# Optimization experiments

Measured on AMD Instinct MI355X. Metric: run time of the kernel, lower is better.

## Reference

```python
import jax, jax.numpy as jnp
import numpy as np

B, T, C = 2, 512, 128
H = 4 * C
EPS_LN = 1e-5
EPS_WKV = 1e-6


def setup_inputs() -> dict:
    key = jax.random.key(0)
    ks = jax.random.split(key, 12)
    def rn(i, shape, s):
        return jax.random.normal(ks[i], shape, jnp.float32) * s
    return {
        "x": jax.random.normal(ks[0], (B, T, C), jnp.float32),
        "ln1_g": jnp.ones((C,), jnp.float32), "ln1_b": jnp.zeros((C,), jnp.float32),
        "mu": rn(1, (C,), 0.1),
        "Wr": rn(2, (C, C), 0.02), "br": jnp.zeros((C,), jnp.float32),
        "Wk": rn(3, (C, C), 0.02), "bk": jnp.zeros((C,), jnp.float32),
        "Wv": rn(4, (C, C), 0.02), "bv": jnp.zeros((C,), jnp.float32),
        "w_decay": rn(5, (C,), 0.5),
        "Wo": rn(6, (C, C), 0.02), "bo": jnp.zeros((C,), jnp.float32),
        "ln2_g": jnp.ones((C,), jnp.float32), "ln2_b": jnp.zeros((C,), jnp.float32),
        "W1": rn(7, (C, H), 0.02), "b1": jnp.zeros((H,), jnp.float32),
        "W2": rn(8, (H, C), 0.02), "b2": jnp.zeros((C,), jnp.float32),
    }


def _ln(x, g, b):
    m = x.mean(-1, keepdims=True)
    v = ((x - m) ** 2).mean(-1, keepdims=True)
    return (x - m) * jax.lax.rsqrt(v + EPS_LN) * g + b


def _wkv_dir(k, v, w_lc):
    # k, v: (B,T,C); w_lc: (T,C) per-(position,channel) decay weight
    p = k[:, :, None, :] * w_lc[None, None, :, :]              # (B,T,L,C)
    p = jnp.exp(p - jax.lax.stop_gradient(p.max(-1, keepdims=True)))  # stable, max over C (as in source, dim=-1)
    p = p / (p.sum(-1, keepdims=True) + EPS_WKV)               # normalize over channel dim, as written in torch
    return jnp.einsum('btlc,blc->btc', p, v)


def _forward(x, ln1_g, ln1_b, mu, Wr, br, Wk, bk, Wv, bv, w_decay, Wo, bo, ln2_g, ln2_b, W1, b1, W2, b2):
    Tn = x.shape[1]
    h = _ln(x, ln1_g, ln1_b)
    # TemporalShift: past half shifted right, future half shifted left
    xp, xf = jnp.split(h, 2, axis=-1)
    xp = jnp.pad(xp, ((0, 0), (1, 0), (0, 0)))[:, :-1]
    xf = jnp.pad(xf, ((0, 0), (0, 1), (0, 0)))[:, 1:]
    hs = h + mu * jnp.concatenate([xp, xf], axis=-1)
    r = jax.nn.sigmoid(hs @ Wr + br)
    k = hs @ Wk + bk
    v = hs @ Wv + bv
    t = jnp.arange(Tn, dtype=x.dtype)[:, None]                 # (T,1)
    neg_w = -jnp.exp(w_decay)[None, :]                         # (1,C)
    w_f = neg_w * (Tn - 1 - t) / (Tn - 1)                      # (T,C)
    w_b = neg_w * t / (Tn - 1)                                 # (T,C)
    x_f = _wkv_dir(k, v, w_f)
    x_b = jnp.flip(_wkv_dir(jnp.flip(k, 1), jnp.flip(v, 1), w_b), 1)
    wk = r * (x_f + x_b) * 0.5
    y = x + wk @ Wo + bo
    h2 = _ln(y, ln2_g, ln2_b)
    m = jax.nn.gelu(h2 @ W1 + b1, approximate=False) @ W2 + b2
    return y + m


def reference(x, ln1_g, ln1_b, mu, Wr, br, Wk, bk, Wv, bv, w_decay, Wo, bo, ln2_g, ln2_b, W1, b1, W2, b2):
    return _forward(x, ln1_g, ln1_b, mu, Wr, br, Wk, bk, Wv, bv, w_decay, Wo, bo, ln2_g, ln2_b, W1, b1, W2, b2)
```

## Files before the change

kernel.cpp:

```cpp
#include <hip/hip_runtime.h>
#include <hip/hip_bf16.h>

#define Bq 2
#define Tq 512
#define Cq 128
#define Hq 512
#define NROW (Bq*Tq)

__device__ __forceinline__ float bfbits2f(unsigned short u) {
    return __uint_as_float(((unsigned)u) << 16);
}
__device__ __forceinline__ bool detect_f32(const void* sent) {
    return *(const unsigned*)sent == 0x3F800000u;
}
#define LD(p, i) (f32 ? ((const float*)(p))[i] : bfbits2f(((const unsigned short*)(p))[i]))
__device__ __forceinline__ float4 LD4(const void* p, int i, bool f32) {
    if (f32) return ((const float4*)p)[i >> 2];
    ushort4 u = *(const ushort4*)((const unsigned short*)p + i);
    return make_float4(bfbits2f(u.x), bfbits2f(u.y), bfbits2f(u.z), bfbits2f(u.w));
}

__global__ __launch_bounds__(512) void kA_qkv(
    const void* __restrict__ sent,
    const void* __restrict__ x,
    const void* __restrict__ ln1g, const void* __restrict__ ln1b,
    const void* __restrict__ mu,
    const void* __restrict__ Wr, const void* __restrict__ br,
    const void* __restrict__ Wk, const void* __restrict__ bk,
    const void* __restrict__ Wv, const void* __restrict__ bv,
    const void* __restrict__ wdec,
    float* __restrict__ r_out, float* __restrict__ u_out,
    float* __restrict__ v_out)
{
    const bool f32 = detect_f32(sent);
    int R0 = blockIdx.x * 2, tid = threadIdx.x;
    int g = tid >> 7, col = tid & 127;
    int t0 = R0 & (Tq - 1);
    int bbase = R0 - t0;

    __shared__ float h4[4][Cq];
    __shared__ __align__(16) float hsi[Cq][2];
    __shared__ __align__(16) float part[3][4][Cq][2];
    __shared__ float wred[8][2];

    {
        int t = t0 - 1 + g;
        int tcl = min(max(t, 0), Tq - 1);
        int row = bbase + tcl;
        float xv = LD(x, row * Cq + col);
        float s1 = xv, s2 = xv * xv;
        for (int off = 32; off; off >>= 1) {
            s1 += __shfl_xor(s1, off);
            s2 += __shfl_xor(s2, off);
        }
        int wid = tid >> 6;
        if ((tid & 63) == 0) { wred[wid][0] = s1; wred[wid][1] = s2; }
        __syncthreads();
        float S1 = wred[2 * g][0] + wred[2 * g + 1][0];
        float S2 = wred[2 * g][1] + wred[2 * g + 1][1];
        float m  = S1 * (1.f / Cq);
        float va = S2 * (1.f / Cq) - m * m;
        float rs = rsqrtf(va + 1e-5f);
        h4[g][col] = (xv - m) * rs * LD(ln1g, col) + LD(ln1b, col);
    }
    __syncthreads();

    if (g < 2) {
        int r2 = g, tt = t0 + r2;
        float hv = h4[r2 + 1][col];
        float nb;
        if (col < Cq / 2) nb = (tt > 0)      ? h4[r2][col]     : 0.f;
        else              nb = (tt < Tq - 1) ? h4[r2 + 2][col] : 0.f;
        hsi[col][r2] = hv + LD(mu, col) * nb;
    }
    __syncthreads();

    if (g < 3) {
        const void* W = (g == 0) ? Wr : (g == 1) ? Wk : Wv;
        int ks = (tid >> 5) & 3, j0 = (tid & 31) * 4;
        float a00 = 0.f, a01 = 0.f, a02 = 0.f, a03 = 0.f;
        float a10 = 0.f, a11 = 0.f, a12 = 0.f, a13 = 0.f;
        int c0 = ks * 32;
#pragma unroll 4
        for (int cc = c0; cc < c0 + 32; ++cc) {
            float4 w  = LD4(W, cc * Cq + j0, f32);
            float2 hv = *(const float2*)&hsi[cc][0];
            a00 += hv.x * w.x; a01 += hv.x * w.y; a02 += hv.x * w.z; a03 += hv.x * w.w;
            a10 += hv.y * w.x; a11 += hv.y * w.y; a12 += hv.y * w.z; a13 += hv.y * w.w;
        }
        *(float4*)&part[g][ks][j0][0]     = make_float4(a00, a10, a01, a11);
        *(float4*)&part[g][ks][j0 + 2][0] = make_float4(a02, a12, a03, a13);
    }
    __syncthreads();

    if (g < 3) {
#pragma unroll
        for (int r2 = 0; r2 < 2; ++r2) {
            float a = (part[g][0][col][r2] + part[g][1][col][r2])
                    + (part[g][2][col][r2] + part[g][3][col][r2]);
            int row = R0 + r2;
            if (g == 0) {
                float rr = 1.f / (1.f + __expf(-(a + LD(br, col))));
                r_out[row * Cq + col] = rr;
            } else if (g == 1) {
                float wd = LD(wdec, col);
                wd = fminf(fmaxf(wd, -20.f), 20.f);
                float negw = -__expf(wd);
                float uu = (a + LD(bk, col)) * negw;
                uu = fminf(fmaxf(uu, -30.f), 30.f);
                u_out[row * Cq + col] = uu;
            } else {
                v_out[row * Cq + col] = a + LD(bv, col);
            }
        }
    }
}

__global__ __launch_bounds__(512) void kB_wkv_ffn(
    const void* __restrict__ sent,
    const float* __restrict__ u_in,
    const float* __restrict__ v_in,
    const float* __restrict__ r_in,
    const void* __restrict__ x,
    const void* __restrict__ Wo, const void* __restrict__ bo,
    const void* __restrict__ lng, const void* __restrict__ lnb,
    const void* __restrict__ W1, const void* __restrict__ b1,
    const void* __restrict__ W2, const void* __restrict__ b2,
    void* __restrict__ out)
{
    const bool f32 = detect_f32(sent);
    int R0 = blockIdx.x * 2, tid = threadIdx.x;
    int b = R0 >> 9;
    const float inv511 = 1.f / (float)(Tq - 1);

    __shared__ float u2[2][Cq];
    __shared__ __align__(16) float rinv2[Tq][2];
    __shared__ float part[8][2][Cq];
    __shared__ __align__(16) float wki[Cq][2];
    __shared__ __align__(16) float h2i[Cq][2];
    __shared__ __align__(16) float m1i[Hq][2];
    __shared__ __align__(16) float pbuf[16 * Cq * 2];
    __shared__ float wred[8][2];

    if (tid < 256) u2[tid >> 7][tid & 127] = u_in[(R0 + (tid >> 7)) * Cq + (tid & 127)];
    __syncthreads();

    {
        int l = tid;
        float a = (float)(Tq - 1 - l) * inv511 * 1.44269504f;
#pragma unroll
        for (int r = 0; r < 2; ++r) {
            float s0 = 0.f, s1 = 0.f, s2 = 0.f, s3 = 0.f;
            const float4* uu4 = (const float4*)u2[r];
            for (int cc = 0; cc < Cq / 4; ++cc) {
                float4 uv = uu4[cc];
                s0 += exp2f(a * uv.x);
                s1 += exp2f(a * uv.y);
                s2 += exp2f(a * uv.z);
                s3 += exp2f(a * uv.w);
            }
            rinv2[l][r] = 1.f / ((s0 + s1) + (s2 + s3) + 1e-6f);
        }
    }
    __syncthreads();

    {
        int seg = tid >> 6, cp = tid & 63, c2 = cp * 2;
        float u00 = u2[0][c2], u01 = u2[0][c2 + 1];
        float u10 = u2[1][c2], u11 = u2[1][c2 + 1];
        float jb = (float)(seg * 64);
        float e00 = __expf(u00 * jb * inv511), e01 = __expf(u01 * jb * inv511);
        float e10 = __expf(u10 * jb * inv511), e11 = __expf(u11 * jb * inv511);
        float g00 = __expf(u00 * inv511), g01 = __expf(u01 * inv511);
        float g10 = __expf(u10 * inv511), g11 = __expf(u11 * inv511);
        float G00 = g00 * g00, G01 = g01 * g01, G10 = g10 * g10, G11 = g11 * g11;
        float p00 = 0.f, p01 = 0.f, p10 = 0.f, p11 = 0.f;
        float q00 = 0.f, q01 = 0.f, q10 = 0.f, q11 = 0.f;
        const float2* vb = (const float2*)(v_in + (size_t)b * Tq * Cq) + cp;
        int j0 = seg * 64;
        for (int j = j0; j < j0 + 64; j += 2) {
            int l = (Tq - 1) - j;
            float2 v0 = vb[(size_t)l * 64];
            float2 v1 = vb[(size_t)(l - 1) * 64];
            float2 ra = *(const float2*)&rinv2[l][0];
            float2 rb = *(const float2*)&rinv2[l - 1][0];
            p00 += v0.x * (e00 * ra.x); p01 += v0.y * (e01 * ra.x);
            p10 += v0.x * (e10 * ra.y); p11 += v0.y * (e11 * ra.y);
            q00 += v1.x * ((e00 * g00) * rb.x); q01 += v1.y * ((e01 * g01) * rb.x);
            q10 += v1.x * ((e10 * g10) * rb.y); q11 += v1.y * ((e11 * g11) * rb.y);
            e00 *= G00; e01 *= G01; e10 *= G10; e11 *= G11;
        }
        part[seg][0][c2]     = p00 + q00;
        part[seg][0][c2 + 1] = p01 + q01;
        part[seg][1][c2]     = p10 + q10;
        part[seg][1][c2 + 1] = p11 + q11;
    }
    __syncthreads();

    if (tid < 256) {
        int r = tid >> 7, c = tid & 127;
        float acc = ((part[0][r][c] + part[1][r][c]) + (part[2][r][c] + part[3][r][c]))
                  + ((part[4][r][c] + part[5][r][c]) + (part[6][r][c] + part[7][r][c]));
        wki[c][r] = r_in[(R0 + r) * Cq + c] * acc;
    }
    __syncthreads();

    {
        int ks = tid >> 5, c0 = (tid & 31) * 4;
        float a00 = 0.f, a01 = 0.f, a02 = 0.f, a03 = 0.f;
        float a10 = 0.f, a11 = 0.f, a12 = 0.f, a13 = 0.f;
        int k0 = ks * 8;
#pragma unroll
        for (int cc = k0; cc < k0 + 8; ++cc) {
            float4 w   = LD4(Wo, cc * Cq + c0, f32);
            float2 wk2 = *(const float2*)&wki[cc][0];
            a00 += wk2.x * w.x; a01 += wk2.x * w.y; a02 += wk2.x * w.z; a03 += wk2.x * w.w;
            a10 += wk2.y * w.x; a11 += wk2.y * w.y; a12 += wk2.y * w.z; a13 += wk2.y * w.w;
        }
        *(float4*)&pbuf[(ks * Cq + c0) * 2]     = make_float4(a00, a10, a01, a11);
        *(float4*)&pbuf[(ks * Cq + c0 + 2) * 2] = make_float4(a02, a12, a03, a13);
    }
    __syncthreads();

    float yv = 0.f;
    if (tid < 256) {
        int r = tid >> 7, c = tid & 127;
        float s = 0.f;
#pragma unroll
        for (int ks = 0; ks < 16; ++ks) s += pbuf[(ks * Cq + c) * 2 + r];
        yv = LD(x, (R0 + r) * Cq + c) + s + LD(bo, c);
    }
    {
        float s1 = yv, s2 = yv * yv;
        for (int off = 32; off; off >>= 1) {
            s1 += __shfl_xor(s1, off);
            s2 += __shfl_xor(s2, off);
        }
        int wid = tid >> 6;
        if ((tid & 63) == 0) { wred[wid][0] = s1; wred[wid][1] = s2; }
        __syncthreads();
        if (tid < 256) {
            int r = tid >> 7, c = tid & 127;
            float S1 = wred[2 * r][0] + wred[2 * r + 1][0];
            float S2 = wred[2 * r][1] + wred[2 * r + 1][1];
            float m  = S1 * (1.f / Cq);
            float va = S2 * (1.f / Cq) - m * m;
            float rs = rsqrtf(va + 1e-5f);
            h2i[c][r] = (yv - m) * rs * LD(lng, c) + LD(lnb, c);
        }
    }
    __syncthreads();

    {
        int ks = tid >> 7, j0 = (tid & 127) * 4;
        float a00 = 0.f, a01 = 0.f, a02 = 0.f, a03 = 0.f;
        float a10 = 0.f, a11 = 0.f, a12 = 0.f, a13 = 0.f;
        int c0 = ks * 32;
#pragma unroll 4
        for (int cc = c0; cc < c0 + 32; ++cc) {
            float4 w  = LD4(W1, cc * Hq + j0, f32);
            float2 hv = *(const float2*)&h2i[cc][0];
            a00 += hv.x * w.x; a01 += hv.x * w.y; a02 += hv.x * w.z; a03 += hv.x * w.w;
            a10 += hv.y * w.x; a11 += hv.y * w.y; a12 += hv.y * w.z; a13 += hv.y * w.w;
        }
        *(float4*)&pbuf[(ks * Hq + j0) * 2]     = make_float4(a00, a10, a01, a11);
        *(float4*)&pbuf[(ks * Hq + j0 + 2) * 2] = make_float4(a02, a12, a03, a13);
    }
    __syncthreads();
    {
        int j = tid;
        float bb = LD(b1, j);
        float x0 = ((pbuf[(0 * Hq + j) * 2]     + pbuf[(1 * Hq + j) * 2])
                  + (pbuf[(2 * Hq + j) * 2]     + pbuf[(3 * Hq + j) * 2])) + bb;
        float x1 = ((pbuf[(0 * Hq + j) * 2 + 1] + pbuf[(1 * Hq + j) * 2 + 1])
                  + (pbuf[(2 * Hq + j) * 2 + 1] + pbuf[(3 * Hq + j) * 2 + 1])) + bb;
        m1i[j][0] = 0.5f * x0 * (1.f + erff(x0 * 0.70710678f));
        m1i[j][1] = 0.5f * x1 * (1.f + erff(x1 * 0.70710678f));
    }
    __syncthreads();

    {
        int ks = tid >> 5, c0 = (tid & 31) * 4;
        float a00 = 0.f, a01 = 0.f, a02 = 0.f, a03 = 0.f;
        float a10 = 0.f, a11 = 0.f, a12 = 0.f, a13 = 0.f;
        int h0 = ks * 32;
#pragma unroll 4
        for (int hh = h0; hh < h0 + 32; ++hh) {
            float4 w  = LD4(W2, hh * Cq + c0, f32);
            float2 mv = *(const float2*)&m1i[hh][0];
            a00 += mv.x * w.x; a01 += mv.x * w.y; a02 += mv.x * w.z; a03 += mv.x * w.w;
            a10 += mv.y * w.x; a11 += mv.y * w.y; a12 += mv.y * w.z; a13 += mv.y * w.w;
        }
        __syncthreads();
        *(float4*)&pbuf[(ks * Cq + c0) * 2]     = make_float4(a00, a10, a01, a11);
        *(float4*)&pbuf[(ks * Cq + c0 + 2) * 2] = make_float4(a02, a12, a03, a13);
    }
    __syncthreads();
    if (tid < 256) {
        int r = tid >> 7, c = tid & 127;
        float s = 0.f;
#pragma unroll
        for (int ks = 0; ks < 16; ++ks) s += pbuf[(ks * Cq + c) * 2 + r];
        float val = yv + s + LD(b2, c);
        int idx = (R0 + r) * Cq + c;
        if (f32) ((float*)out)[idx] = val;
        else     ((__hip_bfloat16*)out)[idx] = __float2bfloat16(val);
    }
}

extern "C" void kernel_launch(void* const* d_in, const int* in_sizes, int n_in,
                              void* d_out, int out_size, void* d_ws, size_t ws_size,
                              hipStream_t stream)
{
    const void* x    = d_in[0];
    const void* ln1g = d_in[1];
    const void* ln1b = d_in[2];
    const void* mu   = d_in[3];
    const void* Wr   = d_in[4];
    const void* br   = d_in[5];
    const void* Wk   = d_in[6];
    const void* bk   = d_in[7];
    const void* Wv   = d_in[8];
    const void* bv   = d_in[9];
    const void* wdec = d_in[10];
    const void* Wo   = d_in[11];
    const void* bo   = d_in[12];
    const void* ln2g = d_in[13];
    const void* ln2b = d_in[14];
    const void* W1   = d_in[15];
    const void* b1   = d_in[16];
    const void* W2   = d_in[17];
    const void* b2   = d_in[18];

    float* ws = (float*)d_ws;
    float* u  = ws;
    float* r  = ws + 131072;
    float* v  = ws + 262144;

    kA_qkv<<<NROW / 2, 512, 0, stream>>>(ln1g, x, ln1g, ln1b, mu, Wr, br, Wk, bk, Wv, bv, wdec, r, u, v);
    kB_wkv_ffn<<<NROW / 2, 512, 0, stream>>>(ln1g, u, v, r, x, Wo, bo, ln2g, ln2b, W1, b1, W2, b2, d_out);
}
```

Baseline: 156.3 us.

## Remap WKV work per wavefront to drop block barriers and shuffle-reduce QKV

In the WKV+FFN kernel, each wavefront now loads its own copy of u and computes the normalizer rows (in reversed order) that it later consumes itself. This removes two block-wide barriers. The time-scan loop is unrolled by four, and the r and x loads are issued early so their latency overlaps the scan. In the QKV kernel, the partial-sum shared buffer and one barrier are replaced by a wave-level shuffle reduction with float4 bias and stores, and each wave handles one matrix and one row. The cost is redundant u loads per wave and fewer active waves (6 of 8) in the projection stage.

```diff
diff --git a/kernel.cpp b/kernel.cpp
--- a/kernel.cpp
+++ b/kernel.cpp
@@ -40,7 +40,6 @@
 
     __shared__ float h4[4][Cq];
     __shared__ __align__(16) float hsi[Cq][2];
-    __shared__ __align__(16) float part[3][4][Cq][2];
     __shared__ float wred[8][2];
 
     {
@@ -75,42 +74,66 @@
     }
     __syncthreads();
 
-    if (g < 3) {
-        const void* W = (g == 0) ? Wr : (g == 1) ? Wk : Wv;
-        int ks = (tid >> 5) & 3, j0 = (tid & 31) * 4;
-        float a00 = 0.f, a01 = 0.f, a02 = 0.f, a03 = 0.f;
-        float a10 = 0.f, a11 = 0.f, a12 = 0.f, a13 = 0.f;
-        int c0 = ks * 32;
-#pragma unroll 4
-        for (int cc = c0; cc < c0 + 32; ++cc) {
-            float4 w  = LD4(W, cc * Cq + j0, f32);
-            float2 hv = *(const float2*)&hsi[cc][0];
-            a00 += hv.x * w.x; a01 += hv.x * w.y; a02 += hv.x * w.z; a03 += hv.x * w.w;
-            a10 += hv.y * w.x; a11 += hv.y * w.y; a12 += hv.y * w.z; a13 += hv.y * w.w;
-        }
-        *(float4*)&part[g][ks][j0][0]     = make_float4(a00, a10, a01, a11);
-        *(float4*)&part[g][ks][j0 + 2][0] = make_float4(a02, a12, a03, a13);
-    }
-    __syncthreads();
-
-    if (g < 3) {
-#pragma unroll
-        for (int r2 = 0; r2 < 2; ++r2) {
-            float a = (part[g][0][col][r2] + part[g][1][col][r2])
-                    + (part[g][2][col][r2] + part[g][3][col][r2]);
-            int row = R0 + r2;
-            if (g == 0) {
-                float rr = 1.f / (1.f + __expf(-(a + LD(br, col))));
-                r_out[row * Cq + col] = rr;
-            } else if (g == 1) {
-                float wd = LD(wdec, col);
-                wd = fminf(fmaxf(wd, -20.f), 20.f);
-                float negw = -__expf(wd);
-                float uu = (a + LD(bk, col)) * negw;
-                uu = fminf(fmaxf(uu, -30.f), 30.f);
-                u_out[row * Cq + col] = uu;
-            } else {
-                v_out[row * Cq + col] = a + LD(bv, col);
+    {
+        int w = tid >> 6, lane = tid & 63;
+        if (w < 6) {
+            int m = w >> 1, r = w & 1;
+            const void* W = (m == 0) ? Wr : (m == 1) ? Wk : Wv;
+            int ks = lane >> 5, j0 = (lane & 31) * 4;
+            float a0 = 0.f, a1 = 0.f, a2 = 0.f, a3 = 0.f;
+            int cbase = ks * 64;
+            for (int cc = cbase; cc < cbase + 64; cc += 4) {
+                float4 w0 = LD4(W, (cc + 0) * Cq + j0, f32);
+                float4 w1 = LD4(W, (cc + 1) * Cq + j0, f32);
+                float4 w2 = LD4(W, (cc + 2) * Cq + j0, f32);
+                float4 w3 = LD4(W, (cc + 3) * Cq + j0, f32);
+                float h0 = hsi[cc + 0][r];
+                float h1 = hsi[cc + 1][r];
+                float h2 = hsi[cc + 2][r];
+                float h3 = hsi[cc + 3][r];
+                a0 += h0 * w0.x; a1 += h0 * w0.y; a2 += h0 * w0.z; a3 += h0 * w0.w;
+                a0 += h1 * w1.x; a1 += h1 * w1.y; a2 += h1 * w1.z; a3 += h1 * w1.w;
+                a0 += h2 * w2.x; a1 += h2 * w2.y; a2 += h2 * w2.z; a3 += h2 * w2.w;
+                a0 += h3 * w3.x; a1 += h3 * w3.y; a2 += h3 * w3.z; a3 += h3 * w3.w;
+            }
+            a0 += __shfl_xor(a0, 32);
+            a1 += __shfl_xor(a1, 32);
+            a2 += __shfl_xor(a2, 32);
+            a3 += __shfl_xor(a3, 32);
+            if (ks == 0) {
+                int row = R0 + r;
+                if (m == 0) {
+                    float4 bb = LD4(br, j0, f32);
+                    float4 o;
+                    o.x = 1.f / (1.f + __expf(-(a0 + bb.x)));
+                    o.y = 1.f / (1.f + __expf(-(a1 + bb.y)));
+                    o.z = 1.f / (1.f + __expf(-(a2 + bb.z)));
+                    o.w = 1.f / (1.f + __expf(-(a3 + bb.w)));
+                    *(float4*)&r_out[row * Cq + j0] = o;
+                } else if (m == 1) {
+                    float4 bb = LD4(bk, j0, f32);
+                    float4 wd = LD4(wdec, j0, f32);
+                    float4 o;
+                    {
+                        float w0c = fminf(fmaxf(wd.x, -20.f), 20.f);
+                        float w1c = fminf(fmaxf(wd.y, -20.f), 20.f);
+                        float w2c = fminf(fmaxf(wd.z, -20.f), 20.f);
+                        float w3c = fminf(fmaxf(wd.w, -20.f), 20.f);
+                        o.x = (a0 + bb.x) * (-__expf(w0c));
+                        o.y = (a1 + bb.y) * (-__expf(w1c));
+                        o.z = (a2 + bb.z) * (-__expf(w2c));
+                        o.w = (a3 + bb.w) * (-__expf(w3c));
+                        o.x = fminf(fmaxf(o.x, -30.f), 30.f);
+                        o.y = fminf(fmaxf(o.y, -30.f), 30.f);
+                        o.z = fminf(fmaxf(o.z, -30.f), 30.f);
+                        o.w = fminf(fmaxf(o.w, -30.f), 30.f);
+                    }
+                    *(float4*)&u_out[row * Cq + j0] = o;
+                } else {
+                    float4 bb = LD4(bv, j0, f32);
+                    float4 o = make_float4(a0 + bb.x, a1 + bb.y, a2 + bb.z, a3 + bb.w);
+                    *(float4*)&v_out[row * Cq + j0] = o;
+                }
             }
         }
     }
@@ -132,6 +155,7 @@
     int R0 = blockIdx.x * 2, tid = threadIdx.x;
     int b = R0 >> 9;
     const float inv511 = 1.f / (float)(Tq - 1);
+    int w = tid >> 6, lane = tid & 63;
 
     __shared__ float u2[2][Cq];
     __shared__ __align__(16) float rinv2[Tq][2];
@@ -142,12 +166,20 @@
     __shared__ __align__(16) float pbuf[16 * Cq * 2];
     __shared__ float wred[8][2];
 
-    if (tid < 256) u2[tid >> 7][tid & 127] = u_in[(R0 + (tid >> 7)) * Cq + (tid & 127)];
-    __syncthreads();
-
-    {
-        int l = tid;
-        float a = (float)(Tq - 1 - l) * inv511 * 1.44269504f;
+    {
+        const float4* us = (const float4*)(u_in + (size_t)R0 * Cq);
+        ((float4*)u2)[lane] = us[lane];
+    }
+    float rv_pre = 0.f, xv_pre = 0.f;
+    if (tid < 256) {
+        int r = tid >> 7, c = tid & 127;
+        rv_pre = r_in[(R0 + r) * Cq + c];
+        xv_pre = LD(x, (R0 + r) * Cq + c);
+    }
+
+    {
+        int l = (Tq - 1) - tid;
+        float a = (float)tid * inv511 * 1.44269504f;
 #pragma unroll
         for (int r = 0; r < 2; ++r) {
             float s0 = 0.f, s1 = 0.f, s2 = 0.f, s3 = 0.f;
@@ -162,38 +194,69 @@
             rinv2[l][r] = 1.f / ((s0 + s1) + (s2 + s3) + 1e-6f);
         }
     }
-    __syncthreads();
-
-    {
-        int seg = tid >> 6, cp = tid & 63, c2 = cp * 2;
+
+    {
+        int c2 = lane * 2;
         float u00 = u2[0][c2], u01 = u2[0][c2 + 1];
         float u10 = u2[1][c2], u11 = u2[1][c2 + 1];
-        float jb = (float)(seg * 64);
+        int j0 = w * 64;
+        float jb = (float)j0;
         float e00 = __expf(u00 * jb * inv511), e01 = __expf(u01 * jb * inv511);
         float e10 = __expf(u10 * jb * inv511), e11 = __expf(u11 * jb * inv511);
         float g00 = __expf(u00 * inv511), g01 = __expf(u01 * inv511);
         float g10 = __expf(u10 * inv511), g11 = __expf(u11 * inv511);
-        float G00 = g00 * g00, G01 = g01 * g01, G10 = g10 * g10, G11 = g11 * g11;
-        float p00 = 0.f, p01 = 0.f, p10 = 0.f, p11 = 0.f;
-        float q00 = 0.f, q01 = 0.f, q10 = 0.f, q11 = 0.f;
-        const float2* vb = (const float2*)(v_in + (size_t)b * Tq * Cq) + cp;
-        int j0 = seg * 64;
-        for (int j = j0; j < j0 + 64; j += 2) {
-            int l = (Tq - 1) - j;
-            float2 v0 = vb[(size_t)l * 64];
-            float2 v1 = vb[(size_t)(l - 1) * 64];
-            float2 ra = *(const float2*)&rinv2[l][0];
-            float2 rb = *(const float2*)&rinv2[l - 1][0];
-            p00 += v0.x * (e00 * ra.x); p01 += v0.y * (e01 * ra.x);
-            p10 += v0.x * (e10 * ra.y); p11 += v0.y * (e11 * ra.y);
-            q00 += v1.x * ((e00 * g00) * rb.x); q01 += v1.y * ((e01 * g01) * rb.x);
-            q10 += v1.x * ((e10 * g10) * rb.y); q11 += v1.y * ((e11 * g11) * rb.y);
-            e00 *= G00; e01 *= G01; e10 *= G10; e11 *= G11;
-        }
-        part[seg][0][c2]     = p00 + q00;
-        part[seg][0][c2 + 1] = p01 + q01;
-        part[seg][1][c2]     = p10 + q10;
-        part[seg][1][c2 + 1] = p11 + q11;
+        float a00 = 0.f, a01 = 0.f, a10 = 0.f, a11 = 0.f;
+        int lhi = (Tq - 1) - j0;
+        const float2* vp = (const float2*)(v_in + (size_t)b * Tq * Cq) + lane + (size_t)lhi * 64;
+        const float2* rp = (const float2*)rinv2 + lhi;
+        for (int it = 0; it < 16; ++it) {
+            float2 v0 = vp[0];
+            float2 v1 = vp[-64];
+            float2 v2 = vp[-128];
+            float2 v3 = vp[-192];
+            float2 r0 = rp[0];
+            float2 r1 = rp[-1];
+            float2 r2 = rp[-2];
+            float2 r3 = rp[-3];
+            {
+                float f1 = e00 * g00, f2 = f1 * g00, f3 = f2 * g00;
+                a00 += v0.x * (e00 * r0.x);
+                a00 += v1.x * (f1 * r1.x);
+                a00 += v2.x * (f2 * r2.x);
+                a00 += v3.x * (f3 * r3.x);
+                e00 = f3 * g00;
+            }
+            {
+                float f1 = e01 * g01, f2 = f1 * g01, f3 = f2 * g01;
+                a01 += v0.y * (e01 * r0.x);
+                a01 += v1.y * (f1 * r1.x);
+                a01 += v2.y * (f2 * r2.x);
+                a01 += v3.y * (f3 * r3.x);
+                e01 = f3 * g01;
+            }
+            {
+                float f1 = e10 * g10, f2 = f1 * g10, f3 = f2 * g10;
+                a10 += v0.x * (e10 * r0.y);
+                a10 += v1.x * (f1 * r1.y);
+                a10 += v2.x * (f2 * r2.y);
+                a10 += v3.x * (f3 * r3.y);
+                e10 = f3 * g10;
+            }
+            {
+                float f1 = e11 * g11, f2 = f1 * g11, f3 = f2 * g11;
+                a11 += v0.y * (e11 * r0.y);
+                a11 += v1.y * (f1 * r1.y);
+                a11 += v2.y * (f2 * r2.y);
+                a11 += v3.y * (f3 * r3.y);
+                e11 = f3 * g11;
+            }
+            vp -= 256;
+            rp -= 4;
+        }
+        part[w][0][c2]     = a00;
+        part[w][0][c2 + 1] = a01;
+        part[w][1][c2]     = a10;
+        part[w][1][c2 + 1] = a11;
     }
     __syncthreads();
 
@@ -201,7 +264,7 @@
         int r = tid >> 7, c = tid & 127;
         float acc = ((part[0][r][c] + part[1][r][c]) + (part[2][r][c] + part[3][r][c]))
                   + ((part[4][r][c] + part[5][r][c]) + (part[6][r][c] + part[7][r][c]));
-        wki[c][r] = r_in[(R0 + r) * Cq + c] * acc;
+        wki[c][r] = rv_pre * acc;
     }
     __syncthreads();
 
@@ -212,10 +275,10 @@
         int k0 = ks * 8;
 #pragma unroll
         for (int cc = k0; cc < k0 + 8; ++cc) {
-            float4 w   = LD4(Wo, cc * Cq + c0, f32);
+            float4 wv   = LD4(Wo, cc * Cq + c0, f32);
             float2 wk2 = *(const float2*)&wki[cc][0];
-            a00 += wk2.x * w.x; a01 += wk2.x * w.y; a02 += wk2.x * w.z; a03 += wk2.x * w.w;
-            a10 += wk2.y * w.x; a11 += wk2.y * w.y; a12 += wk2.y * w.z; a13 += wk2.y * w.w;
+            a00 += wk2.x * wv.x; a01 += wk2.x * wv.y; a02 += wk2.x * wv.z; a03 += wk2.x * wv.w;
+            a10 += wk2.y * wv.x; a11 += wk2.y * wv.y; a12 += wk2.y * wv.z; a13 += wk2.y * wv.w;
         }
         *(float4*)&pbuf[(ks * Cq + c0) * 2]     = make_float4(a00, a10, a01, a11);
         *(float4*)&pbuf[(ks * Cq + c0 + 2) * 2] = make_float4(a02, a12, a03, a13);
@@ -224,11 +287,11 @@
 
     float yv = 0.f;
     if (tid < 256) {
-        int r = tid >> 7, c = tid & 127;
+        int c = tid & 127;
         float s = 0.f;
 #pragma unroll
-        for (int ks = 0; ks < 16; ++ks) s += pbuf[(ks * Cq + c) * 2 + r];
-        yv = LD(x, (R0 + r) * Cq + c) + s + LD(bo, c);
+        for (int ks = 0; ks < 16; ++ks) s += pbuf[(ks * Cq + c) * 2 + (tid >> 7)];
+        yv = xv_pre + s + LD(bo, c);
     }
     {
         float s1 = yv, s2 = yv * yv;
@@ -258,10 +321,10 @@
         int c0 = ks * 32;
 #pragma unroll 4
         for (int cc = c0; cc < c0 + 32; ++cc) {
-            float4 w  = LD4(W1, cc * Hq + j0, f32);
+            float4 wv = LD4(W1, cc * Hq + j0, f32);
             float2 hv = *(const float2*)&h2i[cc][0];
-            a00 += hv.x * w.x; a01 += hv.x * w.y; a02 += hv.x * w.z; a03 += hv.x * w.w;
-            a10 += hv.y * w.x; a11 += hv.y * w.y; a12 += hv.y * w.z; a13 += hv.y * w.w;
+            a00 += hv.x * wv.x; a01 += hv.x * wv.y; a02 += hv.x * wv.z; a03 += hv.x * wv.w;
+            a10 += hv.y * wv.x; a11 += hv.y * wv.y; a12 += hv.y * wv.z; a13 += hv.y * wv.w;
         }
         *(float4*)&pbuf[(ks * Hq + j0) * 2]     = make_float4(a00, a10, a01, a11);
         *(float4*)&pbuf[(ks * Hq + j0 + 2) * 2] = make_float4(a02, a12, a03, a13);
@@ -286,10 +349,10 @@
         int h0 = ks * 32;
 #pragma unroll 4
         for (int hh = h0; hh < h0 + 32; ++hh) {
-            float4 w  = LD4(W2, hh * Cq + c0, f32);
+            float4 wv = LD4(W2, hh * Cq + c0, f32);
             float2 mv = *(const float2*)&m1i[hh][0];
-            a00 += mv.x * w.x; a01 += mv.x * w.y; a02 += mv.x * w.z; a03 += mv.x * w.w;
-            a10 += mv.y * w.x; a11 += mv.y * w.y; a12 += mv.y * w.z; a13 += mv.y * w.w;
+            a00 += mv.x * wv.x; a01 += mv.x * wv.y; a02 += mv.x * wv.z; a03 += mv.x * wv.w;
+            a10 += mv.y * wv.x; a11 += mv.y * wv.y; a12 += mv.y * wv.z; a13 += mv.y * wv.w;
         }
         __syncthreads();
         *(float4*)&pbuf[(ks * Cq + c0) * 2]     = make_float4(a00, a10, a01, a11);
```

New measurement: 149.8 us. -4.2%, faster.
